# Kernel optimization log

Measured on AMD Instinct MI355X. Metric: run time of the kernel, lower is better.

The kernel has to match this reference:

```python
import jax, jax.numpy as jnp
import numpy as np

DIM = 32  # fixed internal node dim
N_GRAPHS = 64


def setup_inputs() -> dict:
    key = jax.random.key(0)
    ks = jax.random.split(key, 16)
    N, E, F_N, F_E, H = 12500, 200000, 16, 8, 32
    inp = {
        "x": jax.random.normal(ks[0], (N, F_N), dtype=jnp.float32),
        "edge_index": jax.random.randint(ks[1], (2, E), 0, N, dtype=jnp.int64),
        "edge_attr": jax.random.normal(ks[2], (E, F_E), dtype=jnp.float32),
        "batch": jnp.sort(jax.random.randint(ks[3], (N,), 0, N_GRAPHS, dtype=jnp.int64)),
        "lin0_w": jax.random.normal(ks[4], (DIM, F_N), dtype=jnp.float32) * 0.1,
        "lin0_b": jax.random.normal(ks[5], (DIM,), dtype=jnp.float32) * 0.1,
        "nn_w": jax.random.normal(ks[6], (DIM * H, F_E), dtype=jnp.float32) * 0.1,
        "nn_b": jax.random.normal(ks[7], (DIM * H,), dtype=jnp.float32) * 0.1,
        "root_w": jax.random.normal(ks[8], (DIM, H), dtype=jnp.float32) * 0.1,
        "conv_b": jax.random.normal(ks[9], (H,), dtype=jnp.float32) * 0.1,
        "lin1_w": jax.random.normal(ks[10], (16, H), dtype=jnp.float32) * 0.1,
        "lin1_b": jax.random.normal(ks[11], (16,), dtype=jnp.float32) * 0.1,
        "lin2_w": jax.random.normal(ks[12], (1, 16), dtype=jnp.float32) * 0.1,
        "lin2_b": jax.random.normal(ks[13], (1,), dtype=jnp.float32) * 0.1,
    }
    return inp


def reference(x, edge_index, edge_attr, batch, lin0_w, lin0_b, nn_w, nn_b,
              root_w, conv_b, lin1_w, lin1_b, lin2_w, lin2_b):
    N = x.shape[0]
    H = conv_b.shape[0]
    # lin0 + relu -> node features [N, DIM]
    out = jax.nn.relu(x @ lin0_w.T + lin0_b)
    # NNConv: per-edge weight matrices from edge MLP (single Linear)
    src, dst = edge_index[0], edge_index[1]
    w_e = (edge_attr @ nn_w.T + nn_b).reshape(-1, DIM, H)  # [E, DIM, H]
    msg = jnp.einsum('ed,edh->eh', out[src], w_e)          # gather + per-edge matmul
    agg = jax.ops.segment_sum(msg, dst, num_segments=N)     # scatter-add
    h = jax.nn.relu(agg + out @ root_w + conv_b)             # root weight + bias
    # global add pool over graphs
    u = jax.ops.segment_sum(h, batch, num_segments=N_GRAPHS)  # [G, H]
    o = jax.nn.relu(u @ lin1_w.T + lin1_b)
    o = o @ lin2_w.T + lin2_b
    return o.reshape(-1)
```

## Files before the change

kernel.cpp:

```cpp
#include <hip/hip_runtime.h>

#define DIMN 32
#define HD   32
#define FN   16
#define FE   8
#define NG   64
#define NPB1 16
#define CAP  64
#define NPW  4

__global__ __launch_bounds__(256) void k1_node_pre(
    const float* __restrict__ x, const float* __restrict__ lin0_w,
    const float* __restrict__ lin0_b, const float* __restrict__ nn_w,
    const float* __restrict__ nn_b,
    float* __restrict__ outn, float* __restrict__ G, float* __restrict__ bmsg,
    float* __restrict__ agg, float* __restrict__ u, int* __restrict__ deg, int N)
{
    __shared__ float s_nnw[DIMN * HD * FE];
    __shared__ float s_nnb[DIMN * HD];
    __shared__ float s_l0w[DIMN * FN];
    __shared__ float s_l0b[DIMN];
    __shared__ float s_out[NPB1 * DIMN];

    const int tid = threadIdx.x;
    for (int i = tid; i < DIMN * HD * FE; i += 256) s_nnw[i] = nn_w[i];
    for (int i = tid; i < DIMN * HD; i += 256)      s_nnb[i] = nn_b[i];
    for (int i = tid; i < DIMN * FN; i += 256)      s_l0w[i] = lin0_w[i];
    if (tid < DIMN) s_l0b[tid] = lin0_b[tid];

    const int n0 = blockIdx.x * NPB1;

    {
        const int a0 = n0 * HD;
        const int a1 = min((n0 + NPB1) * HD, N * HD);
        for (int i = a0 + tid; i < a1; i += 256) agg[i] = 0.f;
        if (tid < NPB1 && n0 + tid < N) deg[n0 + tid] = 0;
        if (blockIdx.x < (NG * HD) / 256) u[blockIdx.x * 256 + tid] = 0.f;
    }
    __syncthreads();

    #pragma unroll
    for (int pass = 0; pass < 2; ++pass) {
        const int nl = pass * 8 + (tid >> 5);
        const int d  = tid & 31;
        const int n  = n0 + nl;
        if (n < N) {
            float s = s_l0b[d];
            const float* xr = x + (size_t)n * FN;
            #pragma unroll
            for (int j = 0; j < FN; ++j) s = fmaf(xr[j], s_l0w[d * FN + j], s);
            s = fmaxf(s, 0.f);
            s_out[nl * DIMN + d] = s;
            outn[(size_t)n * DIMN + d] = s;
        }
    }
    __syncthreads();

    for (int nl = 0; nl < NPB1; ++nl) {
        const int n = n0 + nl;
        if (n >= N) break;
        float g = 0.f;
        #pragma unroll 8
        for (int d = 0; d < DIMN; ++d)
            g = fmaf(s_out[nl * DIMN + d], s_nnw[d * 256 + tid], g);
        G[(size_t)n * 256 + tid] = g;
    }

    #pragma unroll
    for (int pass = 0; pass < 2; ++pass) {
        const int nl = pass * 8 + (tid >> 5);
        const int h  = tid & 31;
        const int n  = n0 + nl;
        if (n < N) {
            float b = 0.f;
            #pragma unroll 8
            for (int d = 0; d < DIMN; ++d)
                b = fmaf(s_out[nl * DIMN + d], s_nnb[d * HD + h], b);
            bmsg[(size_t)n * HD + h] = b;
        }
    }
}

__global__ __launch_bounds__(256) void kb_bucket(
    const int* __restrict__ ei, const float* __restrict__ ea,
    const float* __restrict__ G, const float* __restrict__ bmsg,
    int* __restrict__ deg, int* __restrict__ eidx, float* __restrict__ agg, int E)
{
    const int e = blockIdx.x * 256 + threadIdx.x;
    if (e >= E) return;
    const int dst = ei[E + e];
    const int pos = atomicAdd(&deg[dst], 1);
    if (pos < CAP) {
        eidx[dst * CAP + pos] = e;
    } else {
        const int src = ei[e];
        for (int h = 0; h < HD; ++h) {
            float m = bmsg[(size_t)src * HD + h];
            #pragma unroll
            for (int f = 0; f < FE; ++f)
                m = fmaf(ea[(size_t)e * FE + f], G[(size_t)src * 256 + h * FE + f], m);
            atomicAdd(agg + (size_t)dst * HD + h, m);
        }
    }
}

__global__ __launch_bounds__(256) void k23_gather_upd(
    const int* __restrict__ ei, const float* __restrict__ ea,
    const float* __restrict__ G, const float* __restrict__ bmsg,
    const int* __restrict__ deg, const int* __restrict__ eidx,
    const float* __restrict__ agg, const float* __restrict__ outn,
    const float* __restrict__ root_w, const float* __restrict__ conv_b,
    const int* __restrict__ batch, float* __restrict__ u, int N)
{
    __shared__ float s_rw[DIMN * HD];
    __shared__ float s_cb[HD];
    const int tid = threadIdx.x;
    for (int i = tid; i < DIMN * HD; i += 256) s_rw[i] = root_w[i];
    if (tid < HD) s_cb[tid] = conv_b[tid];
    __syncthreads();

    const int lane  = tid & 63;
    const int h     = lane & 31;
    const int p     = lane >> 5;
    const int wid   = (blockIdx.x * 256 + tid) >> 6;
    const int nbase = wid * NPW;

    float accp  = 0.f;
    int   g_cur = -1;

    for (int i = 0; i < NPW; ++i) {
        const int n = nbase + i;
        if (n >= N) break;

        const int dn = min(deg[n], CAP);
        float acc = 0.f;
        for (int j = p; j < dn; j += 2) {
            const int e   = eidx[n * CAP + j];
            const int src = ei[e];
            const float4 w0 = *(const float4*)(ea + (size_t)e * FE);
            const float4 w1 = *(const float4*)(ea + (size_t)e * FE + 4);
            const float* gp = G + (size_t)src * 256 + h * 8;
            const float4 ga = *(const float4*)(gp);
            const float4 gb = *(const float4*)(gp + 4);
            float m = bmsg[(size_t)src * HD + h];
            m = fmaf(w0.x, ga.x, m);
            m = fmaf(w0.y, ga.y, m);
            m = fmaf(w0.z, ga.z, m);
            m = fmaf(w0.w, ga.w, m);
            m = fmaf(w1.x, gb.x, m);
            m = fmaf(w1.y, gb.y, m);
            m = fmaf(w1.z, gb.z, m);
            m = fmaf(w1.w, gb.w, m);
            acc += m;
        }
        acc += __shfl_xor(acc, 32);

        float v = acc + s_cb[h] + agg[(size_t)n * HD + h];
        const float orow = outn[(size_t)n * DIMN + h];
        #pragma unroll
        for (int k = 0; k < DIMN; ++k)
            v = fmaf(__shfl(orow, k, 32), s_rw[k * HD + h], v);
        v = fmaxf(v, 0.f);

        const int g = batch[n];
        if (g != g_cur) {
            if (g_cur >= 0 && p == 0)
                atomicAdd(u + (size_t)g_cur * HD + h, accp);
            g_cur = g;
            accp = v;
        } else {
            accp += v;
        }
    }
    if (g_cur >= 0 && p == 0)
        atomicAdd(u + (size_t)g_cur * HD + h, accp);
}

__global__ __launch_bounds__(64) void k4_head(
    const float* __restrict__ u, const float* __restrict__ lin1_w,
    const float* __restrict__ lin1_b, const float* __restrict__ lin2_w,
    const float* __restrict__ lin2_b, float* __restrict__ outp)
{
    const int g = threadIdx.x;
    if (g >= NG) return;

    float ur[HD];
    #pragma unroll
    for (int hh = 0; hh < HD; ++hh) ur[hh] = u[(size_t)g * HD + hh];

    float acc = lin2_b[0];
    #pragma unroll
    for (int i = 0; i < 16; ++i) {
        float o = lin1_b[i];
        #pragma unroll
        for (int hh = 0; hh < HD; ++hh)
            o = fmaf(ur[hh], lin1_w[i * HD + hh], o);
        o = fmaxf(o, 0.f);
        acc = fmaf(o, lin2_w[i], acc);
    }
    outp[g] = acc;
}

extern "C" void kernel_launch(void* const* d_in, const int* in_sizes, int n_in,
                              void* d_out, int out_size, void* d_ws, size_t ws_size,
                              hipStream_t stream)
{
    const float* x      = (const float*)d_in[0];
    const int*   ei     = (const int*)  d_in[1];
    const float* ea     = (const float*)d_in[2];
    const int*   batch  = (const int*)  d_in[3];
    const float* lin0_w = (const float*)d_in[4];
    const float* lin0_b = (const float*)d_in[5];
    const float* nn_w   = (const float*)d_in[6];
    const float* nn_b   = (const float*)d_in[7];
    const float* root_w = (const float*)d_in[8];
    const float* conv_b = (const float*)d_in[9];
    const float* lin1_w = (const float*)d_in[10];
    const float* lin1_b = (const float*)d_in[11];
    const float* lin2_w = (const float*)d_in[12];
    const float* lin2_b = (const float*)d_in[13];

    const int N = in_sizes[0] / FN;
    const int E = in_sizes[2] / FE;

    float* ws   = (float*)d_ws;
    float* outn = ws;
    float* G    = outn + (size_t)N * DIMN;
    float* bmsg = G    + (size_t)N * 256;
    float* agg  = bmsg + (size_t)N * DIMN;
    float* u    = agg  + (size_t)N * DIMN;
    int*   deg  = (int*)(u + (size_t)NG * HD);
    int*   eidx = deg + N;

    const int nb1 = (N + NPB1 - 1) / NPB1;
    k1_node_pre<<<nb1, 256, 0, stream>>>(x, lin0_w, lin0_b, nn_w, nn_b,
                                         outn, G, bmsg, agg, u, deg, N);

    const int nbb = (E + 255) / 256;
    kb_bucket<<<nbb, 256, 0, stream>>>(ei, ea, G, bmsg, deg, eidx, agg, E);

    const int nwaves = (N + NPW - 1) / NPW;
    const int nb23   = (nwaves + 3) / 4;
    k23_gather_upd<<<nb23, 256, 0, stream>>>(ei, ea, G, bmsg, deg, eidx, agg,
                                             outn, root_w, conv_b, batch, u, N);

    k4_head<<<1, 64, 0, stream>>>(u, lin1_w, lin1_b, lin2_w, lin2_b, (float*)d_out);
}
```

Measured before the change: 175.9 us.

## Reassociate NNConv message sum to drop per-node G table and fuse head

The per-node G (N×256) and bmsg tables are no longer precomputed. Each destination node now accumulates T[d,f] = Σ out[src,d]·ea[e,f] and S[d] = Σ out[src,d] over its incoming edges, then contracts these once with a transposed nn_w held in shared memory. This removes the large G write and the 8-float-per-edge gather, replacing them with a single-float gather plus wave shuffles. The head MLP is folded into the gather kernel through a last-block-done atomic counter, which saves a launch. Edges past the bucket capacity now recompute the edge weights from nn_w in global memory, and shuffle and LDS traffic per node goes up.

After: 247.1 us. 40.5% more time.

```diff
diff --git a/kernel.cpp b/kernel.cpp
--- a/kernel.cpp
+++ b/kernel.cpp
@@ -5,86 +5,37 @@
 #define FN   16
 #define FE   8
 #define NG   64
-#define NPB1 16
 #define CAP  64
 #define NPW  4
 
-__global__ __launch_bounds__(256) void k1_node_pre(
+__global__ __launch_bounds__(256) void k1_out(
     const float* __restrict__ x, const float* __restrict__ lin0_w,
-    const float* __restrict__ lin0_b, const float* __restrict__ nn_w,
-    const float* __restrict__ nn_b,
-    float* __restrict__ outn, float* __restrict__ G, float* __restrict__ bmsg,
-    float* __restrict__ agg, float* __restrict__ u, int* __restrict__ deg, int N)
-{
-    __shared__ float s_nnw[DIMN * HD * FE];
-    __shared__ float s_nnb[DIMN * HD];
-    __shared__ float s_l0w[DIMN * FN];
-    __shared__ float s_l0b[DIMN];
-    __shared__ float s_out[NPB1 * DIMN];
-
-    const int tid = threadIdx.x;
-    for (int i = tid; i < DIMN * HD * FE; i += 256) s_nnw[i] = nn_w[i];
-    for (int i = tid; i < DIMN * HD; i += 256)      s_nnb[i] = nn_b[i];
-    for (int i = tid; i < DIMN * FN; i += 256)      s_l0w[i] = lin0_w[i];
-    if (tid < DIMN) s_l0b[tid] = lin0_b[tid];
-
-    const int n0 = blockIdx.x * NPB1;
-
-    {
-        const int a0 = n0 * HD;
-        const int a1 = min((n0 + NPB1) * HD, N * HD);
-        for (int i = a0 + tid; i < a1; i += 256) agg[i] = 0.f;
-        if (tid < NPB1 && n0 + tid < N) deg[n0 + tid] = 0;
-        if (blockIdx.x < (NG * HD) / 256) u[blockIdx.x * 256 + tid] = 0.f;
-    }
-    __syncthreads();
-
+    const float* __restrict__ lin0_b,
+    float* __restrict__ outn, float* __restrict__ aggfb, float* __restrict__ u,
+    int* __restrict__ deg, int* __restrict__ done, int N)
+{
+    const int gt = blockIdx.x * 256 + threadIdx.x;
+    if (gt >= N * DIMN) return;
+    const int n = gt >> 5, d = gt & 31;
+
+    float s = lin0_b[d];
+    const float* xr = x + (size_t)n * FN;
+    const float* wr = lin0_w + d * FN;
     #pragma unroll
-    for (int pass = 0; pass < 2; ++pass) {
-        const int nl = pass * 8 + (tid >> 5);
-        const int d  = tid & 31;
-        const int n  = n0 + nl;
-        if (n < N) {
-            float s = s_l0b[d];
-            const float* xr = x + (size_t)n * FN;
-            #pragma unroll
-            for (int j = 0; j < FN; ++j) s = fmaf(xr[j], s_l0w[d * FN + j], s);
-            s = fmaxf(s, 0.f);
-            s_out[nl * DIMN + d] = s;
-            outn[(size_t)n * DIMN + d] = s;
-        }
-    }
-    __syncthreads();
-
-    for (int nl = 0; nl < NPB1; ++nl) {
-        const int n = n0 + nl;
-        if (n >= N) break;
-        float g = 0.f;
-        #pragma unroll 8
-        for (int d = 0; d < DIMN; ++d)
-            g = fmaf(s_out[nl * DIMN + d], s_nnw[d * 256 + tid], g);
-        G[(size_t)n * 256 + tid] = g;
-    }
-
-    #pragma unroll
-    for (int pass = 0; pass < 2; ++pass) {
-        const int nl = pass * 8 + (tid >> 5);
-        const int h  = tid & 31;
-        const int n  = n0 + nl;
-        if (n < N) {
-            float b = 0.f;
-            #pragma unroll 8
-            for (int d = 0; d < DIMN; ++d)
-                b = fmaf(s_out[nl * DIMN + d], s_nnb[d * HD + h], b);
-            bmsg[(size_t)n * HD + h] = b;
-        }
-    }
+    for (int j = 0; j < FN; ++j) s = fmaf(xr[j], wr[j], s);
+    outn[gt] = fmaxf(s, 0.f);
+
+    aggfb[gt] = 0.f;
+    if (d == 0) deg[n] = 0;
+    if (gt < NG * HD) u[gt] = 0.f;
+    if (gt == 0) *done = 0;
 }
 
 __global__ __launch_bounds__(256) void kb_bucket(
     const int* __restrict__ ei, const float* __restrict__ ea,
-    const float* __restrict__ G, const float* __restrict__ bmsg,
-    int* __restrict__ deg, int* __restrict__ eidx, float* __restrict__ agg, int E)
+    const float* __restrict__ outn, const float* __restrict__ nn_w,
+    const float* __restrict__ nn_b,
+    int* __restrict__ deg, int* __restrict__ eidx, float* __restrict__ aggfb, int E)
 {
     const int e = blockIdx.x * 256 + threadIdx.x;
     if (e >= E) return;
@@ -94,35 +45,56 @@
         eidx[dst * CAP + pos] = e;
     } else {
         const int src = ei[e];
+        float ef[FE];
+        #pragma unroll
+        for (int f = 0; f < FE; ++f) ef[f] = ea[(size_t)e * FE + f];
         for (int h = 0; h < HD; ++h) {
-            float m = bmsg[(size_t)src * HD + h];
-            #pragma unroll
-            for (int f = 0; f < FE; ++f)
-                m = fmaf(ea[(size_t)e * FE + f], G[(size_t)src * 256 + h * FE + f], m);
-            atomicAdd(agg + (size_t)dst * HD + h, m);
-        }
-    }
-}
-
-__global__ __launch_bounds__(256) void k23_gather_upd(
+            float m = 0.f;
+            for (int d = 0; d < DIMN; ++d) {
+                float wdh = nn_b[d * HD + h];
+                #pragma unroll
+                for (int f = 0; f < FE; ++f)
+                    wdh = fmaf(ef[f], nn_w[(d * HD + h) * FE + f], wdh);
+                m = fmaf(outn[(size_t)src * DIMN + d], wdh, m);
+            }
+            atomicAdd(aggfb + (size_t)dst * HD + h, m);
+        }
+    }
+}
+
+__global__ __launch_bounds__(256) void k3_gather(
     const int* __restrict__ ei, const float* __restrict__ ea,
-    const float* __restrict__ G, const float* __restrict__ bmsg,
+    const float* __restrict__ outn, const float* __restrict__ nn_w,
+    const float* __restrict__ nn_b, const float* __restrict__ root_w,
+    const float* __restrict__ conv_b,
     const int* __restrict__ deg, const int* __restrict__ eidx,
-    const float* __restrict__ agg, const float* __restrict__ outn,
-    const float* __restrict__ root_w, const float* __restrict__ conv_b,
-    const int* __restrict__ batch, float* __restrict__ u, int N)
-{
+    const float* __restrict__ aggfb, const int* __restrict__ batch,
+    const float* __restrict__ lin1_w, const float* __restrict__ lin1_b,
+    const float* __restrict__ lin2_w, const float* __restrict__ lin2_b,
+    float* __restrict__ u, int* __restrict__ done, float* __restrict__ outp,
+    int N, int nblocks)
+{
+    __shared__ float s_nnw2[DIMN * FE * HD];
+    __shared__ float s_nnb[DIMN * HD];
     __shared__ float s_rw[DIMN * HD];
     __shared__ float s_cb[HD];
+    __shared__ int   s_last;
+
     const int tid = threadIdx.x;
-    for (int i = tid; i < DIMN * HD; i += 256) s_rw[i] = root_w[i];
+    for (int i = tid; i < DIMN * FE * HD; i += 256) {
+        const int d = i >> 8, rem = i & 255, hh = rem >> 3, f = rem & 7;
+        s_nnw2[(d * 8 + f) * 32 + hh] = nn_w[i];
+    }
+    for (int i = tid; i < DIMN * HD; i += 256) s_nnb[i] = nn_b[i];
+    for (int i = tid; i < DIMN * HD; i += 256) s_rw[i]  = root_w[i];
     if (tid < HD) s_cb[tid] = conv_b[tid];
     __syncthreads();
 
-    const int lane  = tid & 63;
-    const int h     = lane & 31;
-    const int p     = lane >> 5;
-    const int wid   = (blockIdx.x * 256 + tid) >> 6;
+    const int l   = tid & 63;
+    const int h   = l & 31;
+    const int p   = l >> 5;
+    const int P16 = p << 4;
+    const int wid = (blockIdx.x * 4) + (tid >> 6);
     const int nbase = wid * NPW;
 
     float accp  = 0.f;
@@ -133,72 +105,91 @@
         if (n >= N) break;
 
         const int dn = min(deg[n], CAP);
+
+        int e_l = 0, s_l = 0;
+        if (l < dn) {
+            e_l = eidx[n * CAP + l];
+            s_l = ei[e_l];
+        }
+
+        float T0 = 0.f, T1 = 0.f, T2 = 0.f, T3 = 0.f, S = 0.f;
+        for (int j = 0; j < dn; ++j) {
+            const int e   = __shfl(e_l, j, 64);
+            const int src = __shfl(s_l, j, 64);
+            const float4 w4 = *(const float4*)(ea + (size_t)e * FE + 4 * p);
+            const float  o  = outn[(size_t)src * DIMN + h];
+            S  += o;
+            T0 = fmaf(o, w4.x, T0);
+            T1 = fmaf(o, w4.y, T1);
+            T2 = fmaf(o, w4.z, T2);
+            T3 = fmaf(o, w4.w, T3);
+        }
+
         float acc = 0.f;
-        for (int j = p; j < dn; j += 2) {
-            const int e   = eidx[n * CAP + j];
-            const int src = ei[e];
-            const float4 w0 = *(const float4*)(ea + (size_t)e * FE);
-            const float4 w1 = *(const float4*)(ea + (size_t)e * FE + 4);
-            const float* gp = G + (size_t)src * 256 + h * 8;
-            const float4 ga = *(const float4*)(gp);
-            const float4 gb = *(const float4*)(gp + 4);
-            float m = bmsg[(size_t)src * HD + h];
-            m = fmaf(w0.x, ga.x, m);
-            m = fmaf(w0.y, ga.y, m);
-            m = fmaf(w0.z, ga.z, m);
-            m = fmaf(w0.w, ga.w, m);
-            m = fmaf(w1.x, gb.x, m);
-            m = fmaf(w1.y, gb.y, m);
-            m = fmaf(w1.z, gb.z, m);
-            m = fmaf(w1.w, gb.w, m);
-            acc += m;
+        #pragma unroll
+        for (int dd = 0; dd < 16; ++dd) {
+            const int d    = P16 + dd;
+            const int base = d * 256 + h;
+            acc = fmaf(__shfl(T0, d,      64), s_nnw2[base + 0 * 32], acc);
+            acc = fmaf(__shfl(T1, d,      64), s_nnw2[base + 1 * 32], acc);
+            acc = fmaf(__shfl(T2, d,      64), s_nnw2[base + 2 * 32], acc);
+            acc = fmaf(__shfl(T3, d,      64), s_nnw2[base + 3 * 32], acc);
+            acc = fmaf(__shfl(T0, 32 + d, 64), s_nnw2[base + 4 * 32], acc);
+            acc = fmaf(__shfl(T1, 32 + d, 64), s_nnw2[base + 5 * 32], acc);
+            acc = fmaf(__shfl(T2, 32 + d, 64), s_nnw2[base + 6 * 32], acc);
+            acc = fmaf(__shfl(T3, 32 + d, 64), s_nnw2[base + 7 * 32], acc);
+        }
+        #pragma unroll
+        for (int dd = 0; dd < 16; ++dd) {
+            const int d = P16 + dd;
+            acc = fmaf(__shfl(S, d, 32), s_nnb[d * 32 + h], acc);
+        }
+        const float orow = outn[(size_t)n * DIMN + h];
+        #pragma unroll
+        for (int dd = 0; dd < 16; ++dd) {
+            const int d = P16 + dd;
+            acc = fmaf(__shfl(orow, d, 32), s_rw[d * 32 + h], acc);
         }
         acc += __shfl_xor(acc, 32);
 
-        float v = acc + s_cb[h] + agg[(size_t)n * HD + h];
-        const float orow = outn[(size_t)n * DIMN + h];
-        #pragma unroll
-        for (int k = 0; k < DIMN; ++k)
-            v = fmaf(__shfl(orow, k, 32), s_rw[k * HD + h], v);
-        v = fmaxf(v, 0.f);
+        const float v = fmaxf(acc + s_cb[h] + aggfb[(size_t)n * HD + h], 0.f);
 
         const int g = batch[n];
         if (g != g_cur) {
-            if (g_cur >= 0 && p == 0)
-                atomicAdd(u + (size_t)g_cur * HD + h, accp);
+            if (g_cur >= 0 && p == 0) atomicAdd(u + (size_t)g_cur * HD + h, accp);
             g_cur = g;
             accp = v;
         } else {
             accp += v;
         }
     }
-    if (g_cur >= 0 && p == 0)
-        atomicAdd(u + (size_t)g_cur * HD + h, accp);
-}
-
-__global__ __launch_bounds__(64) void k4_head(
-    const float* __restrict__ u, const float* __restrict__ lin1_w,
-    const float* __restrict__ lin1_b, const float* __restrict__ lin2_w,
-    const float* __restrict__ lin2_b, float* __restrict__ outp)
-{
-    const int g = threadIdx.x;
-    if (g >= NG) return;
-
-    float ur[HD];
-    #pragma unroll
-    for (int hh = 0; hh < HD; ++hh) ur[hh] = u[(size_t)g * HD + hh];
-
-    float acc = lin2_b[0];
-    #pragma unroll
-    for (int i = 0; i < 16; ++i) {
-        float o = lin1_b[i];
+    if (g_cur >= 0 && p == 0) atomicAdd(u + (size_t)g_cur * HD + h, accp);
+
+    __threadfence();
+    __syncthreads();
+    if (tid == 0) {
+        const int old = atomicAdd(done, 1);
+        s_last = (old == nblocks - 1) ? 1 : 0;
+    }
+    __syncthreads();
+    if (s_last && tid < NG) {
+        const int g = tid;
+        float ur[HD];
         #pragma unroll
         for (int hh = 0; hh < HD; ++hh)
-            o = fmaf(ur[hh], lin1_w[i * HD + hh], o);
-        o = fmaxf(o, 0.f);
-        acc = fmaf(o, lin2_w[i], acc);
-    }
-    outp[g] = acc;
+            ur[hh] = atomicAdd(&u[(size_t)g * HD + hh], 0.f);
+        float acc2 = lin2_b[0];
+        #pragma unroll
+        for (int i = 0; i < 16; ++i) {
+            float o = lin1_b[i];
+            #pragma unroll
+            for (int hh = 0; hh < HD; ++hh)
+                o = fmaf(ur[hh], lin1_w[i * HD + hh], o);
+            o = fmaxf(o, 0.f);
+            acc2 = fmaf(o, lin2_w[i], acc2);
+        }
+        outp[g] = acc2;
+    }
 }
 
 extern "C" void kernel_launch(void* const* d_in, const int* in_sizes, int n_in,
@@ -223,26 +214,23 @@
     const int N = in_sizes[0] / FN;
     const int E = in_sizes[2] / FE;
 
-    float* ws   = (float*)d_ws;
-    float* outn = ws;
-    float* G    = outn + (size_t)N * DIMN;
-    float* bmsg = G    + (size_t)N * 256;
-    float* agg  = bmsg + (size_t)N * DIMN;
-    float* u    = agg  + (size_t)N * DIMN;
-    int*   deg  = (int*)(u + (size_t)NG * HD);
-    int*   eidx = deg + N;
-
-    const int nb1 = (N + NPB1 - 1) / NPB1;
-    k1_node_pre<<<nb1, 256, 0, stream>>>(x, lin0_w, lin0_b, nn_w, nn_b,
-                                         outn, G, bmsg, agg, u, deg, N);
+    float* ws    = (float*)d_ws;
+    float* outn  = ws;
+    float* aggfb = outn  + (size_t)N * DIMN;
+    float* u     = aggfb + (size_t)N * DIMN;
+    int*   deg   = (int*)(u + (size_t)NG * HD);
+    int*   eidx  = deg + N;
+    int*   done  = eidx + (size_t)N * CAP;
+
+    const int nb1 = (N * DIMN + 255) / 256;
+    k1_out<<<nb1, 256, 0, stream>>>(x, lin0_w, lin0_b, outn, aggfb, u, deg, done, N);
 
     const int nbb = (E + 255) / 256;
-    kb_bucket<<<nbb, 256, 0, stream>>>(ei, ea, G, bmsg, deg, eidx, agg, E);
-
-    const int nwaves = (N + NPW - 1) / NPW;
-    const int nb23   = (nwaves + 3) / 4;
-    k23_gather_upd<<<nb23, 256, 0, stream>>>(ei, ea, G, bmsg, deg, eidx, agg,
-                                             outn, root_w, conv_b, batch, u, N);
-
-    k4_head<<<1, 64, 0, stream>>>(u, lin1_w, lin1_b, lin2_w, lin2_b, (float*)d_out);
-}
+    kb_bucket<<<nbb, 256, 0, stream>>>(ei, ea, outn, nn_w, nn_b, deg, eidx, aggfb, E);
+
+    const int nb3 = (N + NPW * 4 - 1) / (NPW * 4);
+    k3_gather<<<nb3, 256, 0, stream>>>(ei, ea, outn, nn_w, nn_b, root_w, conv_b,
+                                       deg, eidx, aggfb, batch,
+                                       lin1_w, lin1_b, lin2_w, lin2_b,
+                                       u, done, (float*)d_out, N, nb3);
+}
```
